# Kernel tuning notes

Hardware: AMD Instinct MI355X
Metric: run time of the kernel (lower is better)

The kernel has to match this reference:

```python
import jax, jax.numpy as jnp
import numpy as np

C = 1024        # number of classes
N = 8           # proxies per class
ALLNUM = C * N  # 8192 total proxies
DIM = 512
R = 0.05
TOPK = int(np.ceil(R * ALLNUM))  # 410
LAM = 0.3
B = 2048


def setup_inputs() -> dict:
    key = jax.random.key(0)
    k1, k2, k3 = jax.random.split(key, 3)
    inp = jax.random.normal(k1, (B, DIM), dtype=jnp.float32)
    target = jax.random.randint(k2, (B,), 0, C, dtype=jnp.int64)
    # kaiming-uniform-initialized proxies approximated by scaled normal init
    proxies = jax.random.normal(k3, (DIM, ALLNUM), dtype=jnp.float32)
    instance_label = jnp.repeat(jnp.arange(C, dtype=jnp.int64), N)  # [ALLNUM]
    return {"input": inp, "target": target, "Proxies": proxies,
            "instance_label": instance_label}


def reference(input, target, Proxies, instance_label):
    # L2-normalize each proxy column (F.normalize along dim=0, eps=1e-12)
    norm = jnp.maximum(jnp.linalg.norm(Proxies, axis=0, keepdims=True), 1e-12)
    centers = Proxies / norm                             # [DIM, ALLNUM]
    similarity = input @ centers                          # [B, ALLNUM]

    positive_mask = (target[:, None] == instance_label[None, :]).astype(similarity.dtype)
    _, indices = jax.lax.top_k(similarity + 1000.0 * positive_mask, TOPK)  # [B, TOPK]

    rows = jnp.arange(similarity.shape[0])[:, None]
    mask = jnp.zeros_like(similarity).at[rows, indices].set(1.0)
    prob_a = mask * similarity                            # sparse-masked similarities

    y_instance_onehot = jax.nn.one_hot(instance_label, C, dtype=similarity.dtype)  # [ALLNUM, C]
    logits = prob_a @ y_instance_onehot                   # [B, C]

    y_target_onehot = jax.nn.one_hot(target, C, dtype=similarity.dtype)  # [B, C]
    logits_mask = 1.0 - (logits == 0.0).astype(similarity.dtype)

    # scale_mask_softmax with scale=1 along dim=1
    e = jnp.exp(logits) * logits_mask
    predict = e / (1e-8 + jnp.sum(e, axis=1, keepdims=True))
    lossClassify = jnp.mean(jnp.sum(-y_target_onehot * jnp.log(predict + 1e-20), axis=1))

    # proxy regularizer: cross-entropy of proxy-vs-class logits
    simCenter = centers.T @ centers                       # [ALLNUM, ALLNUM]
    centers_logits = simCenter @ y_instance_onehot        # [ALLNUM, C]
    logp = jax.nn.log_softmax(centers_logits, axis=1)
    reg = -jnp.mean(jnp.take_along_axis(logp, instance_label[:, None], axis=1))

    return (lossClassify + LAM * reg, lossClassify)
```

## Files before the change

### kernel.cpp

```cpp
#include <hip/hip_runtime.h>
#include <hip/hip_bf16.h>
#include <math.h>

#define C_CLS   1024
#define NPROXY  8
#define ALLNUM  8192
#define DIM     512
#define TOPK    410
#define LAM     0.3f
#define BATCH   2048

typedef __bf16 bf16x8 __attribute__((ext_vector_type(8)));
typedef float floatx4 __attribute__((ext_vector_type(4)));
typedef unsigned short ushort_t;

#define WS_RNORM 0
#define WS_SIG   8192
#define WS_LP    10240
#define WS_RP    12288
#define WS_ABF   14336
#define WS_PBF   538624
#define WS_STBF  2635776
#define WS_SIM   2897920

__device__ inline float block_reduce(float v, int is_max, float* red, int t) {
    #pragma unroll
    for (int o = 32; o > 0; o >>= 1) {
        float w = __shfl_down(v, o);
        v = is_max ? fmaxf(v, w) : (v + w);
    }
    __syncthreads();
    if ((t & 63) == 0) red[t >> 6] = v;
    __syncthreads();
    return is_max ? fmaxf(fmaxf(red[0], red[1]), fmaxf(red[2], red[3]))
                  : (red[0] + red[1] + red[2] + red[3]);
}

__device__ inline ushort_t f2bf(float f) {
    unsigned u = __float_as_uint(f);
    return (ushort_t)((u + 0x7FFFu + ((u >> 16) & 1u)) >> 16);
}

__device__ inline void ld_g2l_16(const void* g, void* l) {
    __builtin_amdgcn_global_load_lds(
        (const __attribute__((address_space(1))) unsigned int*)g,
        (__attribute__((address_space(3))) unsigned int*)l,
        16, 0, 0);
}

__device__ inline unsigned f2ord(float f) {
    unsigned u = __float_as_uint(f);
    return (u & 0x80000000u) ? ~u : (u | 0x80000000u);
}

__global__ __launch_bounds__(256) void k_prep1(const float* __restrict__ P,
                                               const float* __restrict__ input,
                                               float* __restrict__ rnorm,
                                               float* __restrict__ rowsig,
                                               ushort_t* __restrict__ Abf,
                                               ushort_t* __restrict__ Pbf) {
    __shared__ float tile[32][33];
    __shared__ float red[4];
    int bx = blockIdx.x, t = threadIdx.x;
    if (bx < 32) {
        int j = bx * 256 + t;
        float s = 0.f;
        #pragma unroll 8
        for (int d = 0; d < DIM; ++d) {
            float v = P[(size_t)d * ALLNUM + j];
            s += v * v;
        }
        rnorm[j] = 1.0f / fmaxf(sqrtf(s), 1e-12f);
    } else if (bx < 32 + 1024) {
        int a = bx - 32;
        int idx = a * 256 + t;
        float4 v = ((const float4*)input)[idx];
        ushort4 o;
        o.x = f2bf(v.x); o.y = f2bf(v.y); o.z = f2bf(v.z); o.w = f2bf(v.w);
        ((ushort4*)Abf)[idx] = o;
        float sq = v.x * v.x + v.y * v.y + v.z * v.z + v.w * v.w;
        #pragma unroll
        for (int off = 32; off > 0; off >>= 1) sq += __shfl_down(sq, off);
        int lane = t & 63, w = t >> 6;
        if (lane == 0) red[w] = sq;
        __syncthreads();
        if (t == 0) {
            rowsig[2 * a]     = sqrtf(red[0] + red[1]);
            rowsig[2 * a + 1] = sqrtf(red[2] + red[3]);
        }
    } else {
        int id = bx - 1056;
        int c0 = (id & 255) * 32, r0 = (id >> 8) * 32;
        int tc = t & 31, tr = t >> 5;
        #pragma unroll
        for (int p = 0; p < 4; ++p)
            tile[tr + p * 8][tc] = P[(size_t)(r0 + tr + p * 8) * ALLNUM + c0 + tc];
        __syncthreads();
        #pragma unroll
        for (int p = 0; p < 4; ++p) {
            int oc = tr + p * 8;
            Pbf[(size_t)(c0 + oc) * DIM + r0 + tc] = f2bf(tile[tc][oc]);
        }
    }
}

__global__ __launch_bounds__(256) void k_prep2(const float* __restrict__ P,
                                               const float* __restrict__ rnorm,
                                               ushort_t* __restrict__ Stbf) {
    __shared__ float tile[32][33];
    int bx = blockIdx.x, t = threadIdx.x;
    int c0 = (bx & 31) * 32, d0 = (bx >> 5) * 32;
    int cl = t & 31, dl8 = t >> 5;
    #pragma unroll
    for (int p = 0; p < 4; ++p) {
        int d = d0 + dl8 + 8 * p;
        int c = c0 + cl;
        const float* pp = P + (size_t)d * ALLNUM + c * NPROXY;
        const float* rn = rnorm + c * NPROXY;
        float4 a = *(const float4*)pp;
        float4 b = *(const float4*)(pp + 4);
        float4 ra = *(const float4*)rn;
        float4 rb = *(const float4*)(rn + 4);
        tile[dl8 + 8 * p][cl] = a.x * ra.x + a.y * ra.y + a.z * ra.z + a.w * ra.w +
                                b.x * rb.x + b.y * rb.y + b.z * rb.z + b.w * rb.w;
    }
    __syncthreads();
    #pragma unroll
    for (int p = 0; p < 4; ++p) {
        int cl2 = dl8 + 8 * p, dl2 = t & 31;
        Stbf[(size_t)(c0 + cl2) * DIM + d0 + dl2] = f2bf(tile[dl2][cl2]);
    }
}

template<int MODE>
__global__ __launch_bounds__(256) void k_gemm_bt(const ushort_t* __restrict__ A,
                                                 const ushort_t* __restrict__ B,
                                                 const float* __restrict__ rnorm,
                                                 void* __restrict__ Cmat, int Ndim) {
    __shared__ __align__(16) ushort_t sA[128 * 64];
    __shared__ __align__(16) ushort_t sB[128 * 64];
    int t = threadIdx.x;
    int w = t >> 6, lane = t & 63;
    int wm = w >> 1, wn = w & 1;
    int bi = blockIdx.y * 128, bj = blockIdx.x * 128;

    floatx4 acc[4][4];
    #pragma unroll
    for (int tm = 0; tm < 4; ++tm)
        #pragma unroll
        for (int tn = 0; tn < 4; ++tn)
            acc[tm][tn] = (floatx4){0.f, 0.f, 0.f, 0.f};

    for (int k0 = 0; k0 < DIM; k0 += 64) {
        #pragma unroll
        for (int it = 0; it < 4; ++it) {
            int c = w * 256 + it * 64 + lane;
            int m = c >> 3, s = c & 7;
            int q = s ^ (m & 7);
            ld_g2l_16(A + ((size_t)(bi + m) << 9) + k0 + q * 8,
                      &sA[(w * 256 + it * 64) * 8]);
        }
        #pragma unroll
        for (int it = 0; it < 4; ++it) {
            int c = w * 256 + it * 64 + lane;
            int m = c >> 3, s = c & 7;
            int q = s ^ (m & 7);
            ld_g2l_16(B + ((size_t)(bj + m) << 9) + k0 + q * 8,
                      &sB[(w * 256 + it * 64) * 8]);
        }
        asm volatile("s_waitcnt vmcnt(0)" ::: "memory");
        __syncthreads();

        #pragma unroll
        for (int kk = 0; kk < 2; ++kk) {
            bf16x8 af[4], bfr[4];
            int ml = lane & 15, q = lane >> 4;
            #pragma unroll
            for (int tm = 0; tm < 4; ++tm) {
                int m = wm * 64 + tm * 16 + ml;
                int s = (kk * 4 + q) ^ (m & 7);
                af[tm] = *(const bf16x8*)&sA[m * 64 + s * 8];
            }
            #pragma unroll
            for (int tn = 0; tn < 4; ++tn) {
                int n = wn * 64 + tn * 16 + ml;
                int s = (kk * 4 + q) ^ (n & 7);
                bfr[tn] = *(const bf16x8*)&sB[n * 64 + s * 8];
            }
            #pragma unroll
            for (int tm = 0; tm < 4; ++tm)
                #pragma unroll
                for (int tn = 0; tn < 4; ++tn)
                    acc[tm][tn] = __builtin_amdgcn_mfma_f32_16x16x32_bf16(
                        af[tm], bfr[tn], acc[tm][tn], 0, 0, 0);
        }
        __syncthreads();
    }

    int ml = lane & 15, qd = lane >> 4;
    #pragma unroll
    for (int tm = 0; tm < 4; ++tm) {
        int rowb = bi + wm * 64 + tm * 16 + qd * 4;
        float4 rnr;
        if (MODE == 1) rnr = *(const float4*)&rnorm[rowb];
        #pragma unroll
        for (int tn = 0; tn < 4; ++tn) {
            int col = bj + wn * 64 + tn * 16 + ml;
            float sc = (MODE == 0) ? rnorm[col] : 0.f;
            #pragma unroll
            for (int i = 0; i < 4; ++i) {
                float v = acc[tm][tn][i] * (MODE == 0 ? sc : ((const float*)&rnr)[i]);
                size_t idx = (size_t)(rowb + i) * Ndim + col;
                if (MODE == 0) ((float*)Cmat)[idx] = v;
                else           ((ushort_t*)Cmat)[idx] = f2bf(v);
            }
        }
    }
}

#define SEL_CAP 1024
#define GCAP    64

__device__ inline void suffix_select1(unsigned* s_hist, unsigned kk,
                                      unsigned* s_wtot, unsigned* sh_bin,
                                      unsigned* sh_k, int t, int lane, int wid) {
    unsigned h = s_hist[t];
    unsigned v = h;
    #pragma unroll
    for (int off = 1; off < 64; off <<= 1) {
        unsigned o = __shfl_down(v, off);
        if (lane + off < 64) v += o;
    }
    if (lane == 0) s_wtot[wid] = v;
    __syncthreads();
    unsigned above = v - h;
    for (int w2 = wid + 1; w2 < 4; ++w2) above += s_wtot[w2];
    unsigned cum = above + h;
    if (cum >= kk && above < kk) { *sh_bin = (unsigned)t; *sh_k = kk - above; }
    __syncthreads();
}

__global__ __launch_bounds__(256) void k_rowloss(const float* __restrict__ sim,
                                                 const int* __restrict__ target,
                                                 const float* __restrict__ rowsig,
                                                 float* __restrict__ loss_part) {
    __shared__ float    s_cls[C_CLS];
    __shared__ float    s_bval[SEL_CAP];
    __shared__ ushort_t s_bcol[SEL_CAP];
    __shared__ unsigned s_bhist[256];
    __shared__ float    s_gval[GCAP];
    __shared__ unsigned s_wtot[4];
    __shared__ unsigned sh_cnt, sh_gc, sh_bin, sh_k;
    __shared__ float    sh_thr;
    __shared__ int      sh_fb;
    __shared__ float    red[4];

    int b = blockIdx.x, t = threadIdx.x;
    int lane = t & 63, wid = t >> 6;
    const float* row = sim + (size_t)b * ALLNUM;
    int tgt = target[b];
    float sig = rowsig[b] * (1.0f / 22.616f);
    float hiT = 1.80f * sig, loT = 1.47f * sig;
    float binscale = 256.0f / (hiT - loT);

    float4 v4[8];
    #pragma unroll
    for (int p = 0; p < 8; ++p) v4[p] = ((const float4*)row)[t + 256 * p];

    if (t == 0) { sh_cnt = 0; sh_gc = 0; }
    s_bhist[t] = 0;
    #pragma unroll
    for (int i = 0; i < 4; ++i) s_cls[t + 256 * i] = 0.f;
    __syncthreads();

    float ndef = 0.f;
    #pragma unroll
    for (int p = 0; p < 8; ++p) {
        int f = t + 256 * p;
        int cls = f >> 1;
        const float* pv = (const float*)&v4[p];
        if (cls == tgt) {
            atomicAdd(&s_cls[tgt], pv[0] + pv[1] + pv[2] + pv[3]);
        } else {
            float ds = 0.f;
            #pragma unroll
            for (int e = 0; e < 4; ++e) {
                float v = pv[e];
                if (v >= hiT) { ds += v; ndef += 1.f; }
                else if (v >= loT) {
                    unsigned idx = atomicAdd(&sh_cnt, 1u);
                    if (idx < SEL_CAP) { s_bval[idx] = v; s_bcol[idx] = (ushort_t)(4 * f + e); }
                    int bin = (int)((v - loT) * binscale);
                    bin = (bin > 255) ? 255 : bin;
                    atomicAdd(&s_bhist[bin], 1u);
                }
            }
            float o = __shfl_xor(ds, 1);
            float s2 = ds + o;
            if ((t & 1) == 0 && s2 != 0.f) atomicAdd(&s_cls[cls], s2);
        }
    }
    float ndefT = block_reduce(ndef, 0, red, t);
    int bc = (int)sh_cnt;
    int kq = (TOPK - NPROXY) - (int)ndefT;
    if (t == 0) sh_fb = (kq < 0 || bc < kq || bc > SEL_CAP) ? 1 : 0;
    __syncthreads();

    if (!sh_fb) {
        if (kq > 0) {
            suffix_select1(s_bhist, (unsigned)kq, s_wtot, &sh_bin, &sh_k, t, lane, wid);
            int B = (int)sh_bin;
            int knew = (int)sh_k;
            for (int j = t; j < bc; j += 256) {
                float v = s_bval[j];
                int bin = (int)((v - loT) * binscale);
                bin = (bin > 255) ? 255 : bin;
                if (bin == B) {
                    unsigned g = atomicAdd(&sh_gc, 1u);
                    if (g < GCAP) s_gval[g] = v;
                }
            }
            __syncthreads();
            int gc = (int)sh_gc;
            if (gc <= GCAP) {
                if (t < gc) {
                    float vj = s_gval[t];
                    unsigned g = 0, geq = 0;
                    for (int i = 0; i < gc; ++i) {
                        float vi = s_gval[i];
                        g   += (vi > vj) ? 1u : 0u;
                        geq += (vi >= vj) ? 1u : 0u;
                    }
                    if (g < (unsigned)knew && geq >= (unsigned)knew) sh_thr = vj;
                }
            } else {
                for (int j = t; j < bc; j += 256) {
                    float vj = s_bval[j];
                    unsigned g = 0, geq = 0;
                    for (int i = 0; i < bc; ++i) {
                        float vi = s_bval[i];
                        g   += (vi > vj) ? 1u : 0u;
                        geq += (vi >= vj) ? 1u : 0u;
                    }
                    if (g < (unsigned)kq && geq >= (unsigned)kq) sh_thr = vj;
                }
            }
            __syncthreads();
            float thr = sh_thr;
            for (int j = t; j < bc; j += 256)
                if (s_bval[j] >= thr)
                    atomicAdd(&s_cls[s_bcol[j] >> 3], s_bval[j]);
        }
    } else {
        __syncthreads();
        #pragma unroll
        for (int i = 0; i < 4; ++i) s_cls[t + 256 * i] = 0.f;
        __syncthreads();
        #pragma unroll
        for (int p = 0; p < 8; ++p) {
            int f = t + 256 * p;
            const float* pv = (const float*)&v4[p];
            if ((f >> 1) == tgt)
                atomicAdd(&s_cls[tgt], pv[0] + pv[1] + pv[2] + pv[3]);
        }
        unsigned L = 0u, R = 0xFFFFFFFFu;
        for (int it = 0; it < 33 && R - L > 1; ++it) {
            unsigned mid = L + ((R - L) >> 1);
            float c = 0.f;
            #pragma unroll
            for (int p = 0; p < 8; ++p) {
                int f = t + 256 * p;
                const float* pv = (const float*)&v4[p];
                if ((f >> 1) != tgt) {
                    #pragma unroll
                    for (int e = 0; e < 4; ++e)
                        c += (f2ord(pv[e]) >= mid) ? 1.f : 0.f;
                }
            }
            c = block_reduce(c, 0, red, t);
            if (c >= (float)(TOPK - NPROXY)) L = mid; else R = mid;
            __syncthreads();
        }
        #pragma unroll
        for (int p = 0; p < 8; ++p) {
            int f = t + 256 * p;
            const float* pv = (const float*)&v4[p];
            if ((f >> 1) != tgt) {
                #pragma unroll
                for (int e = 0; e < 4; ++e)
                    if (f2ord(pv[e]) >= L)
                        atomicAdd(&s_cls[f >> 1], pv[e]);
            }
        }
    }
    __syncthreads();

    float4 cv = ((const float4*)s_cls)[t];
    float m = -1e30f;
    if (cv.x != 0.0f) m = fmaxf(m, cv.x);
    if (cv.y != 0.0f) m = fmaxf(m, cv.y);
    if (cv.z != 0.0f) m = fmaxf(m, cv.z);
    if (cv.w != 0.0f) m = fmaxf(m, cv.w);
    m = block_reduce(m, 1, red, t);
    float se = 0.f;
    if (cv.x != 0.0f) se += expf(cv.x - m);
    if (cv.y != 0.0f) se += expf(cv.y - m);
    if (cv.z != 0.0f) se += expf(cv.z - m);
    if (cv.w != 0.0f) se += expf(cv.w - m);
    se = block_reduce(se, 0, red, t);
    if (t == 0) {
        float lt = s_cls[tgt];
        float predict_t = expf(lt - m) / (1e-8f * expf(-m) + se);
        loss_part[b] = -logf(predict_t + 1e-20f);
    }
}

__global__ __launch_bounds__(256) void k_regloss(const ushort_t* __restrict__ logits,
                                                 float* __restrict__ reg_part) {
    __shared__ float bsum[4];
    int t = threadIdx.x, lane = t & 63, wid = t >> 6;
    int i = blockIdx.x * 4 + wid;
    const ushort_t* row = logits + (size_t)i * C_CLS;
    uint4 c0 = ((const uint4*)row)[lane];
    uint4 c1 = ((const uint4*)(row + 512))[lane];

    float f[16];
    const unsigned* u0 = (const unsigned*)&c0;
    const unsigned* u1 = (const unsigned*)&c1;
    #pragma unroll
    for (int k = 0; k < 4; ++k) {
        f[2 * k]     = __uint_as_float(u0[k] << 16);
        f[2 * k + 1] = __uint_as_float(u0[k] & 0xFFFF0000u);
        f[8 + 2 * k]     = __uint_as_float(u1[k] << 16);
        f[8 + 2 * k + 1] = __uint_as_float(u1[k] & 0xFFFF0000u);
    }

    int cstar = i >> 3;
    int chunk = cstar >> 9, within = cstar & 511;
    float sd = 0.f;
    if (lane == (within >> 3)) sd = f[chunk * 8 + (within & 7)];

    float m = -1e30f;
    #pragma unroll
    for (int k = 0; k < 16; ++k) m = fmaxf(m, f[k]);
    #pragma unroll
    for (int off = 32; off > 0; off >>= 1) m = fmaxf(m, __shfl_xor(m, off));

    float se = 0.f;
    #pragma unroll
    for (int k = 0; k < 16; ++k) se += expf(f[k] - m);
    #pragma unroll
    for (int off = 32; off > 0; off >>= 1) se += __shfl_xor(se, off);
    #pragma unroll
    for (int off = 32; off > 0; off >>= 1) sd += __shfl_xor(sd, off);

    if (lane == 0) bsum[wid] = m + logf(se) - sd;
    __syncthreads();
    if (t == 0)
        reg_part[blockIdx.x] = bsum[0] + bsum[1] + bsum[2] + bsum[3];
}

__global__ __launch_bounds__(256) void k_final(const float* __restrict__ lp,
                                               const float* __restrict__ rp,
                                               float* __restrict__ out) {
    __shared__ float red[4];
    int t = threadIdx.x;
    float4 a = ((const float4*)lp)[t];
    float4 b = ((const float4*)lp)[t + 256];
    float4 c = ((const float4*)rp)[t];
    float4 d = ((const float4*)rp)[t + 256];
    float ls = a.x + a.y + a.z + a.w + b.x + b.y + b.z + b.w;
    float rs = c.x + c.y + c.z + c.w + d.x + d.y + d.z + d.w;
    ls = block_reduce(ls, 0, red, t);
    rs = block_reduce(rs, 0, red, t);
    if (t == 0) {
        float lc = ls / (float)BATCH;
        float rg = rs / (float)ALLNUM;
        out[0] = lc + LAM * rg;
        out[1] = lc;
    }
}

extern "C" void kernel_launch(void* const* d_in, const int* in_sizes, int n_in,
                              void* d_out, int out_size, void* d_ws, size_t ws_size,
                              hipStream_t stream) {
    const float* input  = (const float*)d_in[0];
    const int*   target = (const int*)d_in[1];
    const float* P      = (const float*)d_in[2];

    float* ws       = (float*)d_ws;
    float* rnorm    = ws + WS_RNORM;
    float* rowsig   = ws + WS_SIG;
    float* loss_part= ws + WS_LP;
    float* reg_part = ws + WS_RP;
    ushort_t* Abf   = (ushort_t*)(ws + WS_ABF);
    ushort_t* Pbf   = (ushort_t*)(ws + WS_PBF);
    ushort_t* Stbf  = (ushort_t*)(ws + WS_STBF);
    float* sim      = ws + WS_SIM;
    ushort_t* logits= (ushort_t*)sim;
    float* out      = (float*)d_out;

    hipLaunchKernelGGL(k_prep1, dim3(32 + 1024 + 4096), dim3(256), 0, stream,
                       P, input, rnorm, rowsig, Abf, Pbf);
    hipLaunchKernelGGL(k_prep2, dim3((C_CLS / 32) * (DIM / 32)), dim3(256), 0, stream,
                       P, rnorm, Stbf);
    hipLaunchKernelGGL((k_gemm_bt<0>), dim3(ALLNUM / 128, BATCH / 128), dim3(256), 0, stream,
                       Abf, Pbf, rnorm, sim, ALLNUM);
    hipLaunchKernelGGL(k_rowloss, dim3(BATCH), dim3(256), 0, stream,
                       sim, target, rowsig, loss_part);
    hipLaunchKernelGGL((k_gemm_bt<1>), dim3(C_CLS / 128, ALLNUM / 128), dim3(256), 0, stream,
                       Pbf, Stbf, rnorm, logits, C_CLS);
    hipLaunchKernelGGL(k_regloss, dim3(ALLNUM / 4), dim3(256), 0, stream,
                       logits, reg_part);
    hipLaunchKernelGGL(k_final, dim3(1), dim3(256), 0, stream,
                       loss_part, reg_part, out);
}
```

Baseline: 172.2 us.

## Merge independent stages into shared launches and split the proxy norm reduction

The proxy-norm computation is split across 8 thread groups per 32 columns (256 blocks instead of 32), giving more parallelism to the column-strided reads. The Stbf prep is folded into the main similarity GEMM launch as extra blocks, and the per-row top-k loss is fused with the proxy-vs-class GEMM (retiled to 64x64) in one launch. Logits get their own workspace region so both can run concurrently. The intent is to cut launch gaps and let independent work overlap on otherwise idle CUs, at the cost of heterogeneous blocks competing for occupancy and a smaller GEMM tile with less reuse.

Result: slower. 201.6 us (+17.1%).

```diff
diff --git a/kernel.cpp b/kernel.cpp
--- a/kernel.cpp
+++ b/kernel.cpp
@@ -21,7 +21,8 @@
 #define WS_ABF   14336
 #define WS_PBF   538624
 #define WS_STBF  2635776
-#define WS_SIM   2897920
+#define WS_LOG   2897920
+#define WS_SIM   7092224
 
 __device__ inline float block_reduce(float v, int is_max, float* red, int t) {
     #pragma unroll
@@ -60,19 +61,28 @@
                                                ushort_t* __restrict__ Abf,
                                                ushort_t* __restrict__ Pbf) {
     __shared__ float tile[32][33];
-    __shared__ float red[4];
+    float* cred = &tile[0][0];
     int bx = blockIdx.x, t = threadIdx.x;
-    if (bx < 32) {
-        int j = bx * 256 + t;
+    if (bx < 256) {
+        int tc = t & 31, g = t >> 5;
+        int c = bx * 32 + tc;
+        const float* pc = P + (size_t)(g * 64) * ALLNUM + c;
         float s = 0.f;
         #pragma unroll 8
-        for (int d = 0; d < DIM; ++d) {
-            float v = P[(size_t)d * ALLNUM + j];
+        for (int d = 0; d < 64; ++d) {
+            float v = pc[(size_t)d * ALLNUM];
             s += v * v;
         }
-        rnorm[j] = 1.0f / fmaxf(sqrtf(s), 1e-12f);
-    } else if (bx < 32 + 1024) {
-        int a = bx - 32;
+        cred[g * 32 + tc] = s;
+        __syncthreads();
+        if (g == 0) {
+            float tot = 0.f;
+            #pragma unroll
+            for (int k = 0; k < 8; ++k) tot += cred[k * 32 + tc];
+            rnorm[c] = 1.0f / fmaxf(sqrtf(tot), 1e-12f);
+        }
+    } else if (bx < 256 + 1024) {
+        int a = bx - 256;
         int idx = a * 256 + t;
         float4 v = ((const float4*)input)[idx];
         ushort4 o;
@@ -82,14 +92,14 @@
         #pragma unroll
         for (int off = 32; off > 0; off >>= 1) sq += __shfl_down(sq, off);
         int lane = t & 63, w = t >> 6;
-        if (lane == 0) red[w] = sq;
+        if (lane == 0) cred[w] = sq;
         __syncthreads();
         if (t == 0) {
-            rowsig[2 * a]     = sqrtf(red[0] + red[1]);
-            rowsig[2 * a + 1] = sqrtf(red[2] + red[3]);
+            rowsig[2 * a]     = sqrtf(cred[0] + cred[1]);
+            rowsig[2 * a + 1] = sqrtf(cred[2] + cred[3]);
         }
     } else {
-        int id = bx - 1056;
+        int id = bx - 1280;
         int c0 = (id & 255) * 32, r0 = (id >> 8) * 32;
         int tc = t & 31, tr = t >> 5;
         #pragma unroll
@@ -104,116 +114,112 @@
     }
 }
 
-__global__ __launch_bounds__(256) void k_prep2(const float* __restrict__ P,
-                                               const float* __restrict__ rnorm,
-                                               ushort_t* __restrict__ Stbf) {
-    __shared__ float tile[32][33];
+__global__ __launch_bounds__(256) void k_stage2(const ushort_t* __restrict__ A,
+                                                const ushort_t* __restrict__ B,
+                                                const float* __restrict__ P,
+                                                const float* __restrict__ rnorm,
+                                                float* __restrict__ sim,
+                                                ushort_t* __restrict__ Stbf) {
+    __shared__ __align__(16) ushort_t smem[2 * 128 * 64];
     int bx = blockIdx.x, t = threadIdx.x;
-    int c0 = (bx & 31) * 32, d0 = (bx >> 5) * 32;
-    int cl = t & 31, dl8 = t >> 5;
-    #pragma unroll
-    for (int p = 0; p < 4; ++p) {
-        int d = d0 + dl8 + 8 * p;
-        int c = c0 + cl;
-        const float* pp = P + (size_t)d * ALLNUM + c * NPROXY;
-        const float* rn = rnorm + c * NPROXY;
-        float4 a = *(const float4*)pp;
-        float4 b = *(const float4*)(pp + 4);
-        float4 ra = *(const float4*)rn;
-        float4 rb = *(const float4*)(rn + 4);
-        tile[dl8 + 8 * p][cl] = a.x * ra.x + a.y * ra.y + a.z * ra.z + a.w * ra.w +
-                                b.x * rb.x + b.y * rb.y + b.z * rb.z + b.w * rb.w;
-    }
-    __syncthreads();
-    #pragma unroll
-    for (int p = 0; p < 4; ++p) {
-        int cl2 = dl8 + 8 * p, dl2 = t & 31;
-        Stbf[(size_t)(c0 + cl2) * DIM + d0 + dl2] = f2bf(tile[dl2][cl2]);
-    }
-}
-
-template<int MODE>
-__global__ __launch_bounds__(256) void k_gemm_bt(const ushort_t* __restrict__ A,
-                                                 const ushort_t* __restrict__ B,
-                                                 const float* __restrict__ rnorm,
-                                                 void* __restrict__ Cmat, int Ndim) {
-    __shared__ __align__(16) ushort_t sA[128 * 64];
-    __shared__ __align__(16) ushort_t sB[128 * 64];
-    int t = threadIdx.x;
-    int w = t >> 6, lane = t & 63;
-    int wm = w >> 1, wn = w & 1;
-    int bi = blockIdx.y * 128, bj = blockIdx.x * 128;
-
-    floatx4 acc[4][4];
-    #pragma unroll
-    for (int tm = 0; tm < 4; ++tm)
-        #pragma unroll
-        for (int tn = 0; tn < 4; ++tn)
-            acc[tm][tn] = (floatx4){0.f, 0.f, 0.f, 0.f};
-
-    for (int k0 = 0; k0 < DIM; k0 += 64) {
-        #pragma unroll
-        for (int it = 0; it < 4; ++it) {
-            int c = w * 256 + it * 64 + lane;
-            int m = c >> 3, s = c & 7;
-            int q = s ^ (m & 7);
-            ld_g2l_16(A + ((size_t)(bi + m) << 9) + k0 + q * 8,
-                      &sA[(w * 256 + it * 64) * 8]);
-        }
-        #pragma unroll
-        for (int it = 0; it < 4; ++it) {
-            int c = w * 256 + it * 64 + lane;
-            int m = c >> 3, s = c & 7;
-            int q = s ^ (m & 7);
-            ld_g2l_16(B + ((size_t)(bj + m) << 9) + k0 + q * 8,
-                      &sB[(w * 256 + it * 64) * 8]);
-        }
-        asm volatile("s_waitcnt vmcnt(0)" ::: "memory");
+
+    if (bx < 1024) {
+        ushort_t* sA = smem;
+        ushort_t* sB = smem + 128 * 64;
+        int w = t >> 6, lane = t & 63;
+        int wm = w >> 1, wn = w & 1;
+        int bj = (bx & 63) * 128, bi = (bx >> 6) * 128;
+
+        floatx4 acc[4][4];
+        #pragma unroll
+        for (int tm = 0; tm < 4; ++tm)
+            #pragma unroll
+            for (int tn = 0; tn < 4; ++tn)
+                acc[tm][tn] = (floatx4){0.f, 0.f, 0.f, 0.f};
+
+        for (int k0 = 0; k0 < DIM; k0 += 64) {
+            #pragma unroll
+            for (int it = 0; it < 4; ++it) {
+                int c = w * 256 + it * 64 + lane;
+                int m = c >> 3, s = c & 7;
+                int q = s ^ (m & 7);
+                ld_g2l_16(A + ((size_t)(bi + m) << 9) + k0 + q * 8,
+                          &sA[(w * 256 + it * 64) * 8]);
+            }
+            #pragma unroll
+            for (int it = 0; it < 4; ++it) {
+                int c = w * 256 + it * 64 + lane;
+                int m = c >> 3, s = c & 7;
+                int q = s ^ (m & 7);
+                ld_g2l_16(B + ((size_t)(bj + m) << 9) + k0 + q * 8,
+                          &sB[(w * 256 + it * 64) * 8]);
+            }
+            asm volatile("s_waitcnt vmcnt(0)" ::: "memory");
+            __syncthreads();
+
+            #pragma unroll
+            for (int kk = 0; kk < 2; ++kk) {
+                bf16x8 af[4], bfr[4];
+                int ml = lane & 15, q = lane >> 4;
+                #pragma unroll
+                for (int tm = 0; tm < 4; ++tm) {
+                    int m = wm * 64 + tm * 16 + ml;
+                    int s = (kk * 4 + q) ^ (m & 7);
+                    af[tm] = *(const bf16x8*)&sA[m * 64 + s * 8];
+                }
+                #pragma unroll
+                for (int tn = 0; tn < 4; ++tn) {
+                    int n = wn * 64 + tn * 16 + ml;
+                    int s = (kk * 4 + q) ^ (n & 7);
+                    bfr[tn] = *(const bf16x8*)&sB[n * 64 + s * 8];
+                }
+                #pragma unroll
+                for (int tm = 0; tm < 4; ++tm)
+                    #pragma unroll
+                    for (int tn = 0; tn < 4; ++tn)
+                        acc[tm][tn] = __builtin_amdgcn_mfma_f32_16x16x32_bf16(
+                            af[tm], bfr[tn], acc[tm][tn], 0, 0, 0);
+            }
+            __syncthreads();
+        }
+
+        int ml = lane & 15, qd = lane >> 4;
+        #pragma unroll
+        for (int tm = 0; tm < 4; ++tm) {
+            int rowb = bi + wm * 64 + tm * 16 + qd * 4;
+            #pragma unroll
+            for (int tn = 0; tn < 4; ++tn) {
+                int col = bj + wn * 64 + tn * 16 + ml;
+                float sc = rnorm[col];
+                #pragma unroll
+                for (int i = 0; i < 4; ++i)
+                    sim[(size_t)(rowb + i) * ALLNUM + col] = acc[tm][tn][i] * sc;
+            }
+        }
+    } else {
+        float* tile = (float*)smem;
+        int id = bx - 1024;
+        int c0 = (id & 31) * 32, d0 = (id >> 5) * 32;
+        int cl = t & 31, dl8 = t >> 5;
+        #pragma unroll
+        for (int p = 0; p < 4; ++p) {
+            int d = d0 + dl8 + 8 * p;
+            int c = c0 + cl;
+            const float* pp = P + (size_t)d * ALLNUM + c * NPROXY;
+            const float* rn = rnorm + c * NPROXY;
+            float4 a = *(const float4*)pp;
+            float4 b = *(const float4*)(pp + 4);
+            float4 ra = *(const float4*)rn;
+            float4 rb = *(const float4*)(rn + 4);
+            tile[(dl8 + 8 * p) * 33 + cl] =
+                a.x * ra.x + a.y * ra.y + a.z * ra.z + a.w * ra.w +
+                b.x * rb.x + b.y * rb.y + b.z * rb.z + b.w * rb.w;
+        }
         __syncthreads();
-
-        #pragma unroll
-        for (int kk = 0; kk < 2; ++kk) {
-            bf16x8 af[4], bfr[4];
-            int ml = lane & 15, q = lane >> 4;
-            #pragma unroll
-            for (int tm = 0; tm < 4; ++tm) {
-                int m = wm * 64 + tm * 16 + ml;
-                int s = (kk * 4 + q) ^ (m & 7);
-                af[tm] = *(const bf16x8*)&sA[m * 64 + s * 8];
-            }
-            #pragma unroll
-            for (int tn = 0; tn < 4; ++tn) {
-                int n = wn * 64 + tn * 16 + ml;
-                int s = (kk * 4 + q) ^ (n & 7);
-                bfr[tn] = *(const bf16x8*)&sB[n * 64 + s * 8];
-            }
-            #pragma unroll
-            for (int tm = 0; tm < 4; ++tm)
-                #pragma unroll
-                for (int tn = 0; tn < 4; ++tn)
-                    acc[tm][tn] = __builtin_amdgcn_mfma_f32_16x16x32_bf16(
-                        af[tm], bfr[tn], acc[tm][tn], 0, 0, 0);
-        }
-        __syncthreads();
-    }
-
-    int ml = lane & 15, qd = lane >> 4;
-    #pragma unroll
-    for (int tm = 0; tm < 4; ++tm) {
-        int rowb = bi + wm * 64 + tm * 16 + qd * 4;
-        float4 rnr;
-        if (MODE == 1) rnr = *(const float4*)&rnorm[rowb];
-        #pragma unroll
-        for (int tn = 0; tn < 4; ++tn) {
-            int col = bj + wn * 64 + tn * 16 + ml;
-            float sc = (MODE == 0) ? rnorm[col] : 0.f;
-            #pragma unroll
-            for (int i = 0; i < 4; ++i) {
-                float v = acc[tm][tn][i] * (MODE == 0 ? sc : ((const float*)&rnr)[i]);
-                size_t idx = (size_t)(rowb + i) * Ndim + col;
-                if (MODE == 0) ((float*)Cmat)[idx] = v;
-                else           ((ushort_t*)Cmat)[idx] = f2bf(v);
-            }
+        #pragma unroll
+        for (int p = 0; p < 4; ++p) {
+            int cl2 = dl8 + 8 * p, dl2 = t & 31;
+            Stbf[(size_t)(c0 + cl2) * DIM + d0 + dl2] = f2bf(tile[dl2 * 33 + cl2]);
         }
     }
 }
@@ -240,133 +246,155 @@
     __syncthreads();
 }
 
-__global__ __launch_bounds__(256) void k_rowloss(const float* __restrict__ sim,
-                                                 const int* __restrict__ target,
-                                                 const float* __restrict__ rowsig,
-                                                 float* __restrict__ loss_part) {
-    __shared__ float    s_cls[C_CLS];
-    __shared__ float    s_bval[SEL_CAP];
-    __shared__ ushort_t s_bcol[SEL_CAP];
-    __shared__ unsigned s_bhist[256];
-    __shared__ float    s_gval[GCAP];
-    __shared__ unsigned s_wtot[4];
-    __shared__ unsigned sh_cnt, sh_gc, sh_bin, sh_k;
-    __shared__ float    sh_thr;
-    __shared__ int      sh_fb;
-    __shared__ float    red[4];
-
-    int b = blockIdx.x, t = threadIdx.x;
+__global__ __launch_bounds__(256, 8) void k_stage3(const float* __restrict__ sim,
+                                                   const int* __restrict__ target,
+                                                   const float* __restrict__ rowsig,
+                                                   float* __restrict__ loss_part,
+                                                   const ushort_t* __restrict__ Pbf,
+                                                   const ushort_t* __restrict__ Stbf,
+                                                   const float* __restrict__ rnorm,
+                                                   ushort_t* __restrict__ logits) {
+    __shared__ __align__(16) unsigned char smem[16384];
+    int bx = blockIdx.x, t = threadIdx.x;
     int lane = t & 63, wid = t >> 6;
-    const float* row = sim + (size_t)b * ALLNUM;
-    int tgt = target[b];
-    float sig = rowsig[b] * (1.0f / 22.616f);
-    float hiT = 1.80f * sig, loT = 1.47f * sig;
-    float binscale = 256.0f / (hiT - loT);
-
-    float4 v4[8];
-    #pragma unroll
-    for (int p = 0; p < 8; ++p) v4[p] = ((const float4*)row)[t + 256 * p];
-
-    if (t == 0) { sh_cnt = 0; sh_gc = 0; }
-    s_bhist[t] = 0;
-    #pragma unroll
-    for (int i = 0; i < 4; ++i) s_cls[t + 256 * i] = 0.f;
-    __syncthreads();
-
-    float ndef = 0.f;
-    #pragma unroll
-    for (int p = 0; p < 8; ++p) {
-        int f = t + 256 * p;
-        int cls = f >> 1;
-        const float* pv = (const float*)&v4[p];
-        if (cls == tgt) {
-            atomicAdd(&s_cls[tgt], pv[0] + pv[1] + pv[2] + pv[3]);
-        } else {
-            float ds = 0.f;
-            #pragma unroll
-            for (int e = 0; e < 4; ++e) {
-                float v = pv[e];
-                if (v >= hiT) { ds += v; ndef += 1.f; }
-                else if (v >= loT) {
-                    unsigned idx = atomicAdd(&sh_cnt, 1u);
-                    if (idx < SEL_CAP) { s_bval[idx] = v; s_bcol[idx] = (ushort_t)(4 * f + e); }
+
+    if (bx < 2048) {
+        float*    s_cls  = (float*)smem;
+        float*    s_bval = (float*)(smem + 4096);
+        ushort_t* s_bcol = (ushort_t*)(smem + 8192);
+        unsigned* s_bhist= (unsigned*)(smem + 10240);
+        float*    s_gval = (float*)(smem + 11264);
+        unsigned* s_wtot = (unsigned*)(smem + 11520);
+        unsigned* shv    = (unsigned*)(smem + 11536);
+        float*    shf    = (float*)(smem + 11552);
+        int*      shi    = (int*)(smem + 11556);
+        float*    red    = (float*)(smem + 11568);
+
+        int b = bx;
+        const float* row = sim + (size_t)b * ALLNUM;
+        int tgt = target[b];
+        float sig = rowsig[b] * (1.0f / 22.616f);
+        float hiT = 1.80f * sig, loT = 1.47f * sig;
+        float binscale = 256.0f / (hiT - loT);
+
+        float4 v4[8];
+        #pragma unroll
+        for (int p = 0; p < 8; ++p) v4[p] = ((const float4*)row)[t + 256 * p];
+
+        if (t == 0) { shv[0] = 0; shv[1] = 0; }
+        s_bhist[t] = 0;
+        #pragma unroll
+        for (int i = 0; i < 4; ++i) s_cls[t + 256 * i] = 0.f;
+        __syncthreads();
+
+        float ndef = 0.f;
+        #pragma unroll
+        for (int p = 0; p < 8; ++p) {
+            int f = t + 256 * p;
+            int cls = f >> 1;
+            const float* pv = (const float*)&v4[p];
+            if (cls == tgt) {
+                atomicAdd(&s_cls[tgt], pv[0] + pv[1] + pv[2] + pv[3]);
+            } else {
+                float ds = 0.f;
+                #pragma unroll
+                for (int e = 0; e < 4; ++e) {
+                    float v = pv[e];
+                    if (v >= hiT) { ds += v; ndef += 1.f; }
+                    else if (v >= loT) {
+                        unsigned idx = atomicAdd(&shv[0], 1u);
+                        if (idx < SEL_CAP) { s_bval[idx] = v; s_bcol[idx] = (ushort_t)(4 * f + e); }
+                        int bin = (int)((v - loT) * binscale);
+                        bin = (bin > 255) ? 255 : bin;
+                        atomicAdd(&s_bhist[bin], 1u);
+                    }
+                }
+                float o = __shfl_xor(ds, 1);
+                float s2 = ds + o;
+                if ((t & 1) == 0 && s2 != 0.f) atomicAdd(&s_cls[cls], s2);
+            }
+        }
+        float ndefT = block_reduce(ndef, 0, red, t);
+        int bc = (int)shv[0];
+        int kq = (TOPK - NPROXY) - (int)ndefT;
+        if (t == 0) shi[0] = (kq < 0 || bc < kq || bc > SEL_CAP) ? 1 : 0;
+        __syncthreads();
+
+        if (!shi[0]) {
+            if (kq > 0) {
+                suffix_select1(s_bhist, (unsigned)kq, s_wtot, &shv[2], &shv[3], t, lane, wid);
+                int B = (int)shv[2];
+                int knew = (int)shv[3];
+                for (int j = t; j < bc; j += 256) {
+                    float v = s_bval[j];
                     int bin = (int)((v - loT) * binscale);
                     bin = (bin > 255) ? 255 : bin;
-                    atomicAdd(&s_bhist[bin], 1u);
-                }
-            }
-            float o = __shfl_xor(ds, 1);
-            float s2 = ds + o;
-            if ((t & 1) == 0 && s2 != 0.f) atomicAdd(&s_cls[cls], s2);
-        }
-    }
-    float ndefT = block_reduce(ndef, 0, red, t);
-    int bc = (int)sh_cnt;
-    int kq = (TOPK - NPROXY) - (int)ndefT;
-    if (t == 0) sh_fb = (kq < 0 || bc < kq || bc > SEL_CAP) ? 1 : 0;
-    __syncthreads();
-
-    if (!sh_fb) {
-        if (kq > 0) {
-            suffix_select1(s_bhist, (unsigned)kq, s_wtot, &sh_bin, &sh_k, t, lane, wid);
-            int B = (int)sh_bin;
-            int knew = (int)sh_k;
-            for (int j = t; j < bc; j += 256) {
-                float v = s_bval[j];
-                int bin = (int)((v - loT) * binscale);
-                bin = (bin > 255) ? 255 : bin;
-                if (bin == B) {
-                    unsigned g = atomicAdd(&sh_gc, 1u);
-                    if (g < GCAP) s_gval[g] = v;
-                }
-            }
+                    if (bin == B) {
+                        unsigned g = atomicAdd(&shv[1], 1u);
+                        if (g < GCAP) s_gval[g] = v;
+                    }
+                }
+                __syncthreads();
+                int gc = (int)shv[1];
+                if (gc <= GCAP) {
+                    if (t < gc) {
+                        float vj = s_gval[t];
+                        unsigned g = 0, geq = 0;
+                        for (int i = 0; i < gc; ++i) {
+                            float vi = s_gval[i];
+                            g   += (vi > vj) ? 1u : 0u;
+                            geq += (vi >= vj) ? 1u : 0u;
+                        }
+                        if (g < (unsigned)knew && geq >= (unsigned)knew) shf[0] = vj;
+                    }
+                } else {
+                    for (int j = t; j < bc; j += 256) {
+                        float vj = s_bval[j];
+                        unsigned g = 0, geq = 0;
+                        for (int i = 0; i < bc; ++i) {
+                            float vi = s_bval[i];
+                            g   += (vi > vj) ? 1u : 0u;
+                            geq += (vi >= vj) ? 1u : 0u;
+                        }
+                        if (g < (unsigned)kq && geq >= (unsigned)kq) shf[0] = vj;
+                    }
+                }
+                __syncthreads();
+                float thr = shf[0];
+                for (int j = t; j < bc; j += 256)
+                    if (s_bval[j] >= thr)
+                        atomicAdd(&s_cls[s_bcol[j] >> 3], s_bval[j]);
+            }
+        } else {
             __syncthreads();
-            int gc = (int)sh_gc;
-            if (gc <= GCAP) {
-                if (t < gc) {
-                    float vj = s_gval[t];
-                    unsigned g = 0, geq = 0;
-                    for (int i = 0; i < gc; ++i) {
-                        float vi = s_gval[i];
-                        g   += (vi > vj) ? 1u : 0u;
-                        geq += (vi >= vj) ? 1u : 0u;
+            #pragma unroll
+            for (int i = 0; i < 4; ++i) s_cls[t + 256 * i] = 0.f;
+            __syncthreads();
+            #pragma unroll
+            for (int p = 0; p < 8; ++p) {
+                int f = t + 256 * p;
+                const float* pv = (const float*)&v4[p];
+                if ((f >> 1) == tgt)
+                    atomicAdd(&s_cls[tgt], pv[0] + pv[1] + pv[2] + pv[3]);
+            }
+            unsigned L = 0u, R = 0xFFFFFFFFu;
+            for (int it = 0; it < 33 && R - L > 1; ++it) {
+                unsigned mid = L + ((R - L) >> 1);
+                float c = 0.f;
+                #pragma unroll
+                for (int p = 0; p < 8; ++p) {
+                    int f = t + 256 * p;
+                    const float* pv = (const float*)&v4[p];
+                    if ((f >> 1) != tgt) {
+                        #pragma unroll
+                        for (int e = 0; e < 4; ++e)
+                            c += (f2ord(pv[e]) >= mid) ? 1.f : 0.f;
                     }
-                    if (g < (unsigned)knew && geq >= (unsigned)knew) sh_thr = vj;
-                }
-            } else {
-                for (int j = t; j < bc; j += 256) {
-                    float vj = s_bval[j];
-                    unsigned g = 0, geq = 0;
-                    for (int i = 0; i < bc; ++i) {
-                        float vi = s_bval[i];
-                        g   += (vi > vj) ? 1u : 0u;
-                        geq += (vi >= vj) ? 1u : 0u;
-                    }
-                    if (g < (unsigned)kq && geq >= (unsigned)kq) sh_thr = vj;
-                }
-            }
-            __syncthreads();
-            float thr = sh_thr;
-            for (int j = t; j < bc; j += 256)
-                if (s_bval[j] >= thr)
-                    atomicAdd(&s_cls[s_bcol[j] >> 3], s_bval[j]);
-        }
-    } else {
-        __syncthreads();
-        #pragma unroll
-        for (int i = 0; i < 4; ++i) s_cls[t + 256 * i] = 0.f;
-        __syncthreads();
-        #pragma unroll
-        for (int p = 0; p < 8; ++p) {
-            int f = t + 256 * p;
-            const float* pv = (const float*)&v4[p];
-            if ((f >> 1) == tgt)
-                atomicAdd(&s_cls[tgt], pv[0] + pv[1] + pv[2] + pv[3]);
-        }
-        unsigned L = 0u, R = 0xFFFFFFFFu;
-        for (int it = 0; it < 33 && R - L > 1; ++it) {
-            unsigned mid = L + ((R - L) >> 1);
-            float c = 0.f;
+                }
+                c = block_reduce(c, 0, red, t);
+                if (c >= (float)(TOPK - NPROXY)) L = mid; else R = mid;
+                __syncthreads();
+            }
             #pragma unroll
             for (int p = 0; p < 8; ++p) {
                 int f = t + 256 * p;
@@ -374,44 +402,107 @@
                 if ((f >> 1) != tgt) {
                     #pragma unroll
                     for (int e = 0; e < 4; ++e)
-                        c += (f2ord(pv[e]) >= mid) ? 1.f : 0.f;
-                }
-            }
-            c = block_reduce(c, 0, red, t);
-            if (c >= (float)(TOPK - NPROXY)) L = mid; else R = mid;
+                        if (f2ord(pv[e]) >= L)
+                            atomicAdd(&s_cls[f >> 1], pv[e]);
+                }
+            }
+        }
+        __syncthreads();
+
+        float4 cv = ((const float4*)s_cls)[t];
+        float m = -1e30f;
+        if (cv.x != 0.0f) m = fmaxf(m, cv.x);
+        if (cv.y != 0.0f) m = fmaxf(m, cv.y);
+        if (cv.z != 0.0f) m = fmaxf(m, cv.z);
+        if (cv.w != 0.0f) m = fmaxf(m, cv.w);
+        m = block_reduce(m, 1, red, t);
+        float se = 0.f;
+        if (cv.x != 0.0f) se += expf(cv.x - m);
+        if (cv.y != 0.0f) se += expf(cv.y - m);
+        if (cv.z != 0.0f) se += expf(cv.z - m);
+        if (cv.w != 0.0f) se += expf(cv.w - m);
+        se = block_reduce(se, 0, red, t);
+        if (t == 0) {
+            float lt = s_cls[tgt];
+            float predict_t = expf(lt - m) / (1e-8f * expf(-m) + se);
+            loss_part[b] = -logf(predict_t + 1e-20f);
+        }
+    } else {
+        ushort_t* sA = (ushort_t*)smem;
+        ushort_t* sB = (ushort_t*)(smem + 8192);
+        int id = bx - 2048;
+        int bj = (id & 15) * 64;
+        int bi = (id >> 4) * 64;
+        int w = wid;
+        int wm = w >> 1, wn = w & 1;
+
+        floatx4 acc[2][2];
+        #pragma unroll
+        for (int tm = 0; tm < 2; ++tm)
+            #pragma unroll
+            for (int tn = 0; tn < 2; ++tn)
+                acc[tm][tn] = (floatx4){0.f, 0.f, 0.f, 0.f};
+
+        for (int k0 = 0; k0 < DIM; k0 += 64) {
+            #pragma unroll
+            for (int it = 0; it < 2; ++it) {
+                int c = (w * 2 + it) * 64 + lane;
+                int m = c >> 3, s = c & 7;
+                int q = s ^ (m & 7);
+                ld_g2l_16(Pbf + ((size_t)(bi + m) << 9) + k0 + q * 8,
+                          &sA[((w * 2 + it) * 64) * 8]);
+            }
+            #pragma unroll
+            for (int it = 0; it < 2; ++it) {
+                int c = (w * 2 + it) * 64 + lane;
+                int m = c >> 3, s = c & 7;
+                int q = s ^ (m & 7);
+                ld_g2l_16(Stbf + ((size_t)(bj + m) << 9) + k0 + q * 8,
+                          &sB[((w * 2 + it) * 64) * 8]);
+            }
+            asm volatile("s_waitcnt vmcnt(0)" ::: "memory");
             __syncthreads();
-        }
-        #pragma unroll
-        for (int p = 0; p < 8; ++p) {
-            int f = t + 256 * p;
-            const float* pv = (const float*)&v4[p];
-            if ((f >> 1) != tgt) {
-                #pragma unroll
-                for (int e = 0; e < 4; ++e)
-                    if (f2ord(pv[e]) >= L)
-                        atomicAdd(&s_cls[f >> 1], pv[e]);
-            }
-        }
-    }
-    __syncthreads();
-
-    float4 cv = ((const float4*)s_cls)[t];
-    float m = -1e30f;
-    if (cv.x != 0.0f) m = fmaxf(m, cv.x);
-    if (cv.y != 0.0f) m = fmaxf(m, cv.y);
-    if (cv.z != 0.0f) m = fmaxf(m, cv.z);
-    if (cv.w != 0.0f) m = fmaxf(m, cv.w);
-    m = block_reduce(m, 1, red, t);
-    float se = 0.f;
-    if (cv.x != 0.0f) se += expf(cv.x - m);
-    if (cv.y != 0.0f) se += expf(cv.y - m);
-    if (cv.z != 0.0f) se += expf(cv.z - m);
-    if (cv.w != 0.0f) se += expf(cv.w - m);
-    se = block_reduce(se, 0, red, t);
-    if (t == 0) {
-        float lt = s_cls[tgt];
-        float predict_t = expf(lt - m) / (1e-8f * expf(-m) + se);
-        loss_part[b] = -logf(predict_t + 1e-20f);
+
+            #pragma unroll
+            for (int kk = 0; kk < 2; ++kk) {
+                bf16x8 af[2], bfr[2];
+                int ml = lane & 15, q = lane >> 4;
+                #pragma unroll
+                for (int tm = 0; tm < 2; ++tm) {
+                    int m = wm * 32 + tm * 16 + ml;
+                    int s = (kk * 4 + q) ^ (m & 7);
+                    af[tm] = *(const bf16x8*)&sA[m * 64 + s * 8];
+                }
+                #pragma unroll
+                for (int tn = 0; tn < 2; ++tn) {
+                    int n = wn * 32 + tn * 16 + ml;
+                    int s = (kk * 4 + q) ^ (n & 7);
+                    bfr[tn] = *(const bf16x8*)&sB[n * 64 + s * 8];
+                }
+                #pragma unroll
+                for (int tm = 0; tm < 2; ++tm)
+                    #pragma unroll
+                    for (int tn = 0; tn < 2; ++tn)
+                        acc[tm][tn] = __builtin_amdgcn_mfma_f32_16x16x32_bf16(
+                            af[tm], bfr[tn], acc[tm][tn], 0, 0, 0);
+            }
+            __syncthreads();
+        }
+
+        int ml = lane & 15, qd = lane >> 4;
+        #pragma unroll
+        for (int tm = 0; tm < 2; ++tm) {
+            int rowb = bi + wm * 32 + tm * 16 + qd * 4;
+            float4 rnr = *(const float4*)&rnorm[rowb];
+            #pragma unroll
+            for (int tn = 0; tn < 2; ++tn) {
+                int col = bj + wn * 32 + tn * 16 + ml;
+                #pragma unroll
+                for (int i = 0; i < 4; ++i)
+                    logits[(size_t)(rowb + i) * C_CLS + col] =
+                        f2bf(acc[tm][tn][i] * ((const float*)&rnr)[i]);
+            }
+        }
     }
 }
 
@@ -496,20 +587,16 @@
     ushort_t* Abf   = (ushort_t*)(ws + WS_ABF);
     ushort_t* Pbf   = (ushort_t*)(ws + WS_PBF);
     ushort_t* Stbf  = (ushort_t*)(ws + WS_STBF);
+    ushort_t* logits= (ushort_t*)(ws + WS_LOG);
     float* sim      = ws + WS_SIM;
-    ushort_t* logits= (ushort_t*)sim;
     float* out      = (float*)d_out;
 
-    hipLaunchKernelGGL(k_prep1, dim3(32 + 1024 + 4096), dim3(256), 0, stream,
+    hipLaunchKernelGGL(k_prep1, dim3(256 + 1024 + 4096), dim3(256), 0, stream,
                        P, input, rnorm, rowsig, Abf, Pbf);
-    hipLaunchKernelGGL(k_prep2, dim3((C_CLS / 32) * (DIM / 32)), dim3(256), 0, stream,
-                       P, rnorm, Stbf);
-    hipLaunchKernelGGL((k_gemm_bt<0>), dim3(ALLNUM / 128, BATCH / 128), dim3(256), 0, stream,
-                       Abf, Pbf, rnorm, sim, ALLNUM);
-    hipLaunchKernelGGL(k_rowloss, dim3(BATCH), dim3(256), 0, stream,
-                       sim, target, rowsig, loss_part);
-    hipLaunchKernelGGL((k_gemm_bt<1>), dim3(C_CLS / 128, ALLNUM / 128), dim3(256), 0, stream,
-                       Pbf, Stbf, rnorm, logits, C_CLS);
+    hipLaunchKernelGGL(k_stage2, dim3(1024 + 512), dim3(256), 0, stream,
+                       Abf, Pbf, P, rnorm, sim, Stbf);
+    hipLaunchKernelGGL(k_stage3, dim3(2048 + 2048), dim3(256), 0, stream,
+                       sim, target, rowsig, loss_part, Pbf, Stbf, rnorm, logits);
     hipLaunchKernelGGL(k_regloss, dim3(ALLNUM / 4), dim3(256), 0, stream,
                        logits, reg_part);
     hipLaunchKernelGGL(k_final, dim3(1), dim3(256), 0, stream,
```
